# Kernel tuning notes

Measured on AMD Instinct MI355X. Metric: run time of the kernel, lower is better.

The kernel has to match this reference:

```python
import jax, jax.numpy as jnp
import numpy as np

HIDDEN = 1024
OUT = 16

def setup_inputs() -> dict:
    key = jax.random.key(0)
    ks = jax.random.split(key, 12)
    bs, hl, hf = 256, 256, 32
    T, ad = 64, 16
    flat = hl * hf
    s = lambda fi, fo: 1.0 / np.sqrt(fi)
    return {
        "history": jax.random.normal(ks[0], (bs, hl, hf), jnp.float32),
        "action": jax.random.normal(ks[1], (bs, T, ad), jnp.float32),
        # carry-init Dense layers (c and h)
        "Wc": jax.random.normal(ks[2], (flat, HIDDEN), jnp.float32) * s(flat, HIDDEN),
        "bc": jnp.zeros((HIDDEN,), jnp.float32),
        "Wh": jax.random.normal(ks[3], (flat, HIDDEN), jnp.float32) * s(flat, HIDDEN),
        "bh": jnp.zeros((HIDDEN,), jnp.float32),
        # LSTM cell: gates ordered [i, f, g, o]; input dense has no bias (flax LSTMCell)
        "Wi": jax.random.normal(ks[4], (ad, 4 * HIDDEN), jnp.float32) * s(ad, HIDDEN),
        "Wr": jax.random.normal(ks[5], (HIDDEN, 4 * HIDDEN), jnp.float32) * s(HIDDEN, HIDDEN),
        "bg": jnp.zeros((4 * HIDDEN,), jnp.float32),
        # output projection
        "Wo": jax.random.normal(ks[6], (HIDDEN, OUT), jnp.float32) * s(HIDDEN, OUT),
        "bo": jnp.zeros((OUT,), jnp.float32),
    }


def reference(history, action, Wc, bc, Wh, bh, Wi, Wr, bg, Wo, bo):
    bs = history.shape[0]
    flat = history.reshape(bs, -1)
    c0 = jax.nn.relu(flat @ Wc + bc)  # [bs, H]
    h0 = jax.nn.relu(flat @ Wh + bh)  # [bs, H]

    # precompute input contribution to gates for all steps: [T, bs, 4H]
    xg = jnp.einsum('bta,ag->tbg', action, Wi)

    def step(carry, xg_t):
        c, h = carry
        g = xg_t + h @ Wr + bg  # [bs, 4H]
        i, f, gg, o = jnp.split(g, 4, axis=-1)
        c = jax.nn.sigmoid(f) * c + jax.nn.sigmoid(i) * jnp.tanh(gg)
        h = jax.nn.sigmoid(o) * jnp.tanh(c)
        return (c, h), h

    _, hs = jax.lax.scan(step, (c0, h0), xg)  # hs: [T, bs, H]
    x = jnp.transpose(hs, (1, 0, 2))  # [bs, T, H]
    # Dropout is deterministic (identity)
    return x @ Wo + bo  # [bs, T, OUT]
```

## Files before the change

### kernel.cpp

```cpp
#include <hip/hip_runtime.h>
#include <math.h>

#define BS      256
#define FLAT    8192
#define H       1024
#define G4      4096
#define T_STEPS 64
#define AD      16
#define NOUT    16

typedef __attribute__((ext_vector_type(8))) short    bf16x8;
typedef __attribute__((ext_vector_type(4))) float    f32x4;
typedef __attribute__((ext_vector_type(8))) unsigned short u16x8;
typedef __attribute__((ext_vector_type(4))) unsigned short u16x4;

__device__ __forceinline__ float sigf(float x) { return 1.0f / (1.0f + __expf(-x)); }
__device__ __forceinline__ float tanh_fast(float x) {
    float a = fabsf(x);
    float e = __expf(-2.0f * a);
    float r = (1.0f - e) / (1.0f + e);
    return copysignf(r, x);
}
__device__ __forceinline__ unsigned short f2bf(float x) {
    unsigned int u = __float_as_uint(x);
    unsigned int r = (u + 0x7FFFu + ((u >> 16) & 1u)) >> 16;
    return (unsigned short)r;
}
__device__ __forceinline__ float bf2f(unsigned short u) {
    return __uint_as_float(((unsigned int)u) << 16);
}

#define OFF_WRP  (1u<<20)
#define OFF_WIP  (OFF_WRP + (8u<<20))
#define OFF_BGP  (OFF_WIP + (256u<<10))
#define OFF_HPA  (OFF_BGP + (16u<<10))
#define OFF_HPB  (OFF_HPA + (512u<<10))
#define OFF_HS   (OFF_HPB + (512u<<10))
#define OFF_PART (OFF_HS + 48u*BS*H*2u)

__global__ __launch_bounds__(256) void pack_wr(const float* __restrict__ Wr,
                                               unsigned short* __restrict__ Wp)
{
    int g  = blockIdx.x * 256 + threadIdx.x;
    int l  = g & 63;
    int nt = (g >> 6) & 3;
    int kc = (g >> 8) & 31;
    int nb = g >> 13;
    int col   = nt * 1024 + nb * 16 + (l & 15);
    int kbase = kc * 32 + (l >> 4) * 8;
    u16x8 o;
    #pragma unroll
    for (int i = 0; i < 8; ++i)
        o[i] = f2bf(Wr[(size_t)(kbase + i) * G4 + col]);
    *(u16x8*)&Wp[(size_t)g * 8] = o;
}

__global__ __launch_bounds__(256) void pack_wi(const float* __restrict__ Wi,
                                               unsigned short* __restrict__ Wp)
{
    int g  = blockIdx.x * 256 + threadIdx.x;
    int l  = g & 63;
    int nt = (g >> 6) & 3;
    int nb = g >> 8;
    int col   = nt * 1024 + nb * 16 + (l & 15);
    int kbase = (l >> 4) * 8;
    u16x8 o;
    #pragma unroll
    for (int i = 0; i < 8; ++i)
        o[i] = (kbase + i < AD) ? f2bf(Wi[(size_t)(kbase + i) * G4 + col]) : (unsigned short)0;
    *(u16x8*)&Wp[(size_t)g * 8] = o;
}

__global__ __launch_bounds__(256) void pack_bg(const float* __restrict__ bg,
                                               float* __restrict__ bgp)
{
    int t = blockIdx.x * 256 + threadIdx.x;
    int jj = t & 15, nt = (t >> 4) & 3, nb = t >> 6;
    bgp[t] = bg[nt * 1024 + nb * 16 + jj];
}

__global__ __launch_bounds__(256) void init_gemm_sk(
    const float* __restrict__ hist,
    const float* __restrict__ Wc, const float* __restrict__ Wh,
    float* __restrict__ partial)
{
    __shared__ float sA[32 * 34];
    __shared__ float sB[32 * 64];

    const int wg  = blockIdx.x;
    const int ks  = wg >> 8;
    const int mat = (wg >> 7) & 1;
    const int m   = wg & 127;
    const int r0  = (m >> 4) * 32;
    const int cc0 = (m & 15) * 64;
    const float* W = mat ? Wh : Wc;

    const int tid = threadIdx.x;
    const int tx  = tid & 15;
    const int ty  = tid >> 4;

    float acc[2][4] = {};
    const int kend = ks * 2048 + 2048;
    for (int k0 = ks * 2048; k0 < kend; k0 += 32) {
        {
            int kk = tid & 31, rr = tid >> 5;
            #pragma unroll
            for (int it = 0; it < 4; ++it) {
                int row = rr + it * 8;
                sA[kk * 34 + row] = hist[(size_t)(r0 + row) * FLAT + k0 + kk];
            }
        }
        {
            int col = tid & 63, kq = tid >> 6;
            #pragma unroll
            for (int it = 0; it < 8; ++it) {
                int k = kq + it * 4;
                sB[k * 64 + col] = W[(size_t)(k0 + k) * H + cc0 + col];
            }
        }
        __syncthreads();
        #pragma unroll
        for (int kk = 0; kk < 32; ++kk) {
            const float2 a2 = *(const float2*)&sA[kk * 34 + ty * 2];
            const float4 b4 = *(const float4*)&sB[kk * 64 + tx * 4];
            acc[0][0] = fmaf(a2.x, b4.x, acc[0][0]);
            acc[0][1] = fmaf(a2.x, b4.y, acc[0][1]);
            acc[0][2] = fmaf(a2.x, b4.z, acc[0][2]);
            acc[0][3] = fmaf(a2.x, b4.w, acc[0][3]);
            acc[1][0] = fmaf(a2.y, b4.x, acc[1][0]);
            acc[1][1] = fmaf(a2.y, b4.y, acc[1][1]);
            acc[1][2] = fmaf(a2.y, b4.z, acc[1][2]);
            acc[1][3] = fmaf(a2.y, b4.w, acc[1][3]);
        }
        __syncthreads();
    }

    float* dst = partial + (size_t)(ks * 2 + mat) * BS * H;
    #pragma unroll
    for (int i = 0; i < 2; ++i) {
        float4 o = { acc[i][0], acc[i][1], acc[i][2], acc[i][3] };
        *(float4*)&dst[(size_t)(r0 + ty * 2 + i) * H + cc0 + tx * 4] = o;
    }
}

__global__ __launch_bounds__(256) void reduce_pack(
    const float* __restrict__ partial,
    const float* __restrict__ bc, const float* __restrict__ bh,
    float* __restrict__ cbuf, unsigned short* __restrict__ hp0)
{
    int e = blockIdx.x * 256 + threadIdx.x;
    int mat = e >> 18;
    int rc  = e & 0x3FFFF;
    int row = rc >> 10, col = rc & 1023;
    float s = (mat ? bh : bc)[col];
    #pragma unroll
    for (int ks = 0; ks < 4; ++ks)
        s += partial[((size_t)(ks * 2 + mat) * BS + row) * H + col];
    s = fmaxf(s, 0.f);
    if (mat == 0) {
        cbuf[rc] = s;
    } else {
        int off = (row >> 6) * 65536 + (col >> 5) * 2048 + ((row >> 4) & 3) * 512
                + ((((col >> 3) & 3) << 4) + (row & 15)) * 8 + (col & 7);
        hp0[off] = f2bf(s);
    }
}

__global__ __launch_bounds__(256) void lstm_step(
    const float* __restrict__ act,
    const unsigned short* __restrict__ Wip,
    const unsigned short* __restrict__ Wrp,
    const float* __restrict__ bgp,
    const unsigned short* __restrict__ Aprev,
    unsigned short* __restrict__ Anext,
    float* __restrict__ cbuf,
    unsigned short* __restrict__ hs_t,
    int t)
{
    __shared__ __align__(16) unsigned short sB[2][4096];
    __shared__ __align__(16) unsigned short sAct[64 * 32];

    const int tid = threadIdx.x;
    const int wg  = blockIdx.x;
    const int mb  = wg >> 6;
    const int nb  = wg & 63;
    const int wv  = tid >> 6;
    const int l   = tid & 63;

    {
        int row = tid >> 2, q = tid & 3;
        float4 v = *(const float4*)&act[((size_t)(mb * 64 + row) * T_STEPS + t) * AD + q * 4];
        u16x4 b; b[0] = f2bf(v.x); b[1] = f2bf(v.y); b[2] = f2bf(v.z); b[3] = f2bf(v.w);
        *(u16x4*)&sAct[row * 32 + q * 4] = b;
        u16x4 z = { 0, 0, 0, 0 };
        *(u16x4*)&sAct[row * 32 + 16 + q * 4] = z;
    }

    const u16x8* Bsrc = (const u16x8*)(Wrp + (size_t)nb * 65536);
    {
        u16x8 s0 = Bsrc[tid], s1 = Bsrc[256 + tid];
        *(u16x8*)&sB[0][tid * 8]         = s0;
        *(u16x8*)&sB[0][(256 + tid) * 8] = s1;
    }
    u16x8 stg0 = Bsrc[512 + tid];
    u16x8 stg1 = Bsrc[768 + tid];

    const bf16x8* Asrc = ((const bf16x8*)Aprev) + mb * 8192 + wv * 64 + l;
    bf16x8 a0 = Asrc[0];
    bf16x8 a1 = Asrc[256];

    f32x4 acc[4];
    {
        const bf16x8* WiB = ((const bf16x8*)Wip) + nb * 256;
        bf16x8 wb0 = WiB[0 * 64 + l], wb1 = WiB[1 * 64 + l],
               wb2 = WiB[2 * 64 + l], wb3 = WiB[3 * 64 + l];
        float g0 = bgp[nb * 64 +  0 + (l & 15)];
        float g1 = bgp[nb * 64 + 16 + (l & 15)];
        float g2 = bgp[nb * 64 + 32 + (l & 15)];
        float g3 = bgp[nb * 64 + 48 + (l & 15)];
        acc[0] = (f32x4){ g0, g0, g0, g0 };
        acc[1] = (f32x4){ g1, g1, g1, g1 };
        acc[2] = (f32x4){ g2, g2, g2, g2 };
        acc[3] = (f32x4){ g3, g3, g3, g3 };

        __syncthreads();

        bf16x8 aa = *(const bf16x8*)&sAct[(wv * 16 + (l & 15)) * 32 + (l >> 4) * 8];
        acc[0] = __builtin_amdgcn_mfma_f32_16x16x32_bf16(aa, wb0, acc[0], 0, 0, 0);
        acc[1] = __builtin_amdgcn_mfma_f32_16x16x32_bf16(aa, wb1, acc[1], 0, 0, 0);
        acc[2] = __builtin_amdgcn_mfma_f32_16x16x32_bf16(aa, wb2, acc[2], 0, 0, 0);
        acc[3] = __builtin_amdgcn_mfma_f32_16x16x32_bf16(aa, wb3, acc[3], 0, 0, 0);
    }

    for (int c = 0; c < 16; ++c) {
        const int cb = c & 1;
        bf16x8 bf00 = *(const bf16x8*)&sB[cb][(0 * 64 + l) * 8];
        bf16x8 bf01 = *(const bf16x8*)&sB[cb][(1 * 64 + l) * 8];
        bf16x8 bf02 = *(const bf16x8*)&sB[cb][(2 * 64 + l) * 8];
        bf16x8 bf03 = *(const bf16x8*)&sB[cb][(3 * 64 + l) * 8];
        bf16x8 bf10 = *(const bf16x8*)&sB[cb][(4 * 64 + l) * 8];
        bf16x8 bf11 = *(const bf16x8*)&sB[cb][(5 * 64 + l) * 8];
        bf16x8 bf12 = *(const bf16x8*)&sB[cb][(6 * 64 + l) * 8];
        bf16x8 bf13 = *(const bf16x8*)&sB[cb][(7 * 64 + l) * 8];

        if (c < 15) {
            *(u16x8*)&sB[cb ^ 1][tid * 8]         = stg0;
            *(u16x8*)&sB[cb ^ 1][(256 + tid) * 8] = stg1;
        }
        if (c < 14) {
            stg0 = Bsrc[(c + 2) * 512 + tid];
            stg1 = Bsrc[(c + 2) * 512 + 256 + tid];
        }
        bf16x8 ca0 = a0, ca1 = a1;
        if (c < 15) {
            a0 = Asrc[(2 * (c + 1)) * 256];
            a1 = Asrc[(2 * (c + 1) + 1) * 256];
        }

        acc[0] = __builtin_amdgcn_mfma_f32_16x16x32_bf16(ca0, bf00, acc[0], 0, 0, 0);
        acc[1] = __builtin_amdgcn_mfma_f32_16x16x32_bf16(ca0, bf01, acc[1], 0, 0, 0);
        acc[2] = __builtin_amdgcn_mfma_f32_16x16x32_bf16(ca0, bf02, acc[2], 0, 0, 0);
        acc[3] = __builtin_amdgcn_mfma_f32_16x16x32_bf16(ca0, bf03, acc[3], 0, 0, 0);
        acc[0] = __builtin_amdgcn_mfma_f32_16x16x32_bf16(ca1, bf10, acc[0], 0, 0, 0);
        acc[1] = __builtin_amdgcn_mfma_f32_16x16x32_bf16(ca1, bf11, acc[1], 0, 0, 0);
        acc[2] = __builtin_amdgcn_mfma_f32_16x16x32_bf16(ca1, bf12, acc[2], 0, 0, 0);
        acc[3] = __builtin_amdgcn_mfma_f32_16x16x32_bf16(ca1, bf13, acc[3], 0, 0, 0);

        __syncthreads();
    }

    {
        const int jj   = l & 15;
        const int hid  = nb * 16 + jj;
        const int rowb = mb * 64 + wv * 16 + (l >> 4) * 4;
        const int kc   = nb >> 1;
        const int hgrp = ((nb & 1) << 1) | (jj >> 3);
        const int ii   = jj & 7;
        #pragma unroll
        for (int r = 0; r < 4; ++r) {
            int row = rowb + r;
            float gi = acc[0][r], gf = acc[1][r], gg = acc[2][r], go = acc[3][r];
            size_t off = (size_t)row * H + hid;
            float cv = sigf(gf) * cbuf[off] + sigf(gi) * tanh_fast(gg);
            cbuf[off] = cv;
            float hv = sigf(go) * tanh_fast(cv);
            unsigned short hb = f2bf(hv);
            hs_t[off] = hb;
            size_t poff = (size_t)mb * 65536 + kc * 2048 + wv * 512
                        + (hgrp * 16 + (row & 15)) * 8 + ii;
            Anext[poff] = hb;
        }
    }
}

__global__ __launch_bounds__(256) void out_proj(
    const unsigned short* __restrict__ hs,
    const float* __restrict__ Wo,
    const float* __restrict__ bo,
    float* __restrict__ out)
{
    __shared__ float sWo[H * NOUT];
    const int tid = threadIdx.x;
    for (int idx = tid; idx < H * NOUT; idx += 256) sWo[idx] = Wo[idx];
    __syncthreads();

    const int o    = tid & 15;
    const int pl   = tid >> 4;
    const int pair = blockIdx.x * 16 + pl;
    const int b    = pair >> 6;
    const int t    = pair & 63;
    const unsigned short* hrow = hs + ((size_t)t * BS + b) * H;

    float acc = bo[o];
    for (int k = 0; k < H; k += 8) {
        u16x8 u = *(const u16x8*)&hrow[k];
        #pragma unroll
        for (int j = 0; j < 8; ++j)
            acc = fmaf(bf2f(u[j]), sWo[(k + j) * 16 + o], acc);
    }
    out[(size_t)pair * 16 + o] = acc;
}

extern "C" void kernel_launch(void* const* d_in, const int* in_sizes, int n_in,
                              void* d_out, int out_size, void* d_ws, size_t ws_size,
                              hipStream_t stream)
{
    const float* hist = (const float*)d_in[0];
    const float* act  = (const float*)d_in[1];
    const float* Wc   = (const float*)d_in[2];
    const float* bc   = (const float*)d_in[3];
    const float* Wh   = (const float*)d_in[4];
    const float* bh   = (const float*)d_in[5];
    const float* Wi   = (const float*)d_in[6];
    const float* Wr   = (const float*)d_in[7];
    const float* bg   = (const float*)d_in[8];
    const float* Wo   = (const float*)d_in[9];
    const float* bo   = (const float*)d_in[10];
    float* out = (float*)d_out;

    char* W = (char*)d_ws;
    float*          cbuf = (float*)W;
    unsigned short* Wrp  = (unsigned short*)(W + OFF_WRP);
    unsigned short* Wip  = (unsigned short*)(W + OFF_WIP);
    float*          bgp  = (float*)(W + OFF_BGP);
    unsigned short* hpA  = (unsigned short*)(W + OFF_HPA);
    unsigned short* hpB  = (unsigned short*)(W + OFF_HPB);
    unsigned short* hs   = (unsigned short*)(W + OFF_HS);
    float*          part = (float*)(W + OFF_PART);

    pack_wr<<<dim3(2048), dim3(256), 0, stream>>>(Wr, Wrp);
    pack_wi<<<dim3(64),   dim3(256), 0, stream>>>(Wi, Wip);
    pack_bg<<<dim3(16),   dim3(256), 0, stream>>>(bg, bgp);

    init_gemm_sk<<<dim3(1024), dim3(256), 0, stream>>>(hist, Wc, Wh, part);
    reduce_pack<<<dim3(2048), dim3(256), 0, stream>>>(part, bc, bh, cbuf, hpA);

    for (int t = 0; t < T_STEPS; ++t) {
        const unsigned short* Ap = (t & 1) ? hpB : hpA;
        unsigned short*       An = (t & 1) ? hpA : hpB;
        lstm_step<<<dim3(256), dim3(256), 0, stream>>>(
            act, Wip, Wrp, bgp, Ap, An, cbuf, hs + (size_t)t * BS * H, t);
    }

    out_proj<<<dim3(1024), dim3(256), 0, stream>>>(hs, Wo, bo, out);
}
```

Before: 815.2 us.

## Move init GEMM to bf16 MFMA with packed operands and deepen LSTM A prefetch

Replaces the fp32 FMA split-K init GEMM for the c0/h0 carries with a bf16 MFMA kernel. The history and Wc/Wh operands are first packed into fragment-ordered layouts, and Bwp reuses the hs region because init finishes before the steps write to it. The action input is also pre-packed to bf16 once, so each lstm_step drops its shared-memory staging and one barrier. The step loop is unrolled by two so each parity keeps its own A registers, prefetching two chunks ahead. out_proj now handles four row groups per block. Risks are lower precision in the init GEMM and the extra packing kernels and memory traffic.

```diff
diff --git a/kernel.cpp b/kernel.cpp
--- a/kernel.cpp
+++ b/kernel.cpp
@@ -36,7 +36,9 @@
 #define OFF_HPA  (OFF_BGP + (16u<<10))
 #define OFF_HPB  (OFF_HPA + (512u<<10))
 #define OFF_HS   (OFF_HPB + (512u<<10))
-#define OFF_PART (OFF_HS + 48u*BS*H*2u)
+#define OFF_AHP  (OFF_HS + (32u<<20))
+#define OFF_AXP  (OFF_AHP + (4u<<20))
+#define OFF_PART (OFF_AXP + (1u<<20))
 
 __global__ __launch_bounds__(256) void pack_wr(const float* __restrict__ Wr,
                                                unsigned short* __restrict__ Wp)
@@ -79,95 +81,155 @@
     bgp[t] = bg[nt * 1024 + nb * 16 + jj];
 }
 
-__global__ __launch_bounds__(256) void init_gemm_sk(
-    const float* __restrict__ hist,
-    const float* __restrict__ Wc, const float* __restrict__ Wh,
-    float* __restrict__ partial)
-{
-    __shared__ float sA[32 * 34];
-    __shared__ float sB[32 * 64];
-
+__global__ __launch_bounds__(256) void pack_hist(const float* __restrict__ hist,
+                                                 unsigned short* __restrict__ Ap)
+{
+    int g  = blockIdx.x * 256 + threadIdx.x;
+    int l  = g & 63;
+    int kc = (g >> 6) & 255;
+    int mb = g >> 14;
+    const float* src = hist + (size_t)(mb * 16 + (l & 15)) * FLAT + kc * 32 + (l >> 4) * 8;
+    float4 v0 = *(const float4*)src;
+    float4 v1 = *(const float4*)(src + 4);
+    u16x8 o;
+    o[0]=f2bf(v0.x); o[1]=f2bf(v0.y); o[2]=f2bf(v0.z); o[3]=f2bf(v0.w);
+    o[4]=f2bf(v1.x); o[5]=f2bf(v1.y); o[6]=f2bf(v1.z); o[7]=f2bf(v1.w);
+    *(u16x8*)&Ap[(size_t)g * 8] = o;
+}
+
+__global__ __launch_bounds__(256) void pack_wb(const float* __restrict__ Wc,
+                                               const float* __restrict__ Wh,
+                                               unsigned short* __restrict__ Bp)
+{
+    int g  = blockIdx.x * 256 + threadIdx.x;
+    int l  = g & 63;
+    int kc = (g >> 6) & 255;
+    int nb = g >> 14;
+    const float* src = (nb & 64) ? Wh : Wc;
+    int n = (nb & 63) * 16 + (l & 15);
+    int k = kc * 32 + (l >> 4) * 8;
+    u16x8 o;
+    #pragma unroll
+    for (int i = 0; i < 8; ++i)
+        o[i] = f2bf(src[(size_t)(k + i) * H + n]);
+    *(u16x8*)&Bp[(size_t)g * 8] = o;
+}
+
+__global__ __launch_bounds__(256) void pack_act(const float* __restrict__ act,
+                                                unsigned short* __restrict__ Axp)
+{
+    int g = blockIdx.x * 256 + threadIdx.x;
+    int l = g & 63;
+    int q = (g >> 6) & 15;
+    int t = g >> 10;
+    int row = q * 16 + (l & 15);
+    int kb  = (l >> 4) * 8;
+    u16x8 o;
+    if (kb < AD) {
+        const float* src = act + ((size_t)row * T_STEPS + t) * AD + kb;
+        float4 v0 = *(const float4*)src;
+        float4 v1 = *(const float4*)(src + 4);
+        o[0]=f2bf(v0.x); o[1]=f2bf(v0.y); o[2]=f2bf(v0.z); o[3]=f2bf(v0.w);
+        o[4]=f2bf(v1.x); o[5]=f2bf(v1.y); o[6]=f2bf(v1.z); o[7]=f2bf(v1.w);
+    } else {
+        o = (u16x8){0,0,0,0,0,0,0,0};
+    }
+    *(u16x8*)&Axp[(size_t)g * 8] = o;
+}
+
+__global__ __launch_bounds__(256) void init_gemm_mfma(
+    const unsigned short* __restrict__ Ap,
+    const unsigned short* __restrict__ Bp,
+    float* __restrict__ part)
+{
     const int wg  = blockIdx.x;
-    const int ks  = wg >> 8;
-    const int mat = (wg >> 7) & 1;
-    const int m   = wg & 127;
-    const int r0  = (m >> 4) * 32;
-    const int cc0 = (m & 15) * 64;
-    const float* W = mat ? Wh : Wc;
-
+    const int mb  = wg & 3;
+    const int nbl = (wg >> 2) & 15;
+    const int ks  = wg >> 6;
     const int tid = threadIdx.x;
-    const int tx  = tid & 15;
-    const int ty  = tid >> 4;
-
-    float acc[2][4] = {};
-    const int kend = ks * 2048 + 2048;
-    for (int k0 = ks * 2048; k0 < kend; k0 += 32) {
-        {
-            int kk = tid & 31, rr = tid >> 5;
+    const int wv  = tid >> 6;
+    const int l   = tid & 63;
+    const int wm  = wv & 1;
+    const int wn  = wv >> 1;
+
+    const bf16x8* AV = (const bf16x8*)Ap;
+    const bf16x8* BV = (const bf16x8*)Bp;
+    const int am0 = mb * 4 + wm * 2;
+    const int bn0 = nbl * 8 + wn * 4;
+    const bf16x8* A0 = AV + (size_t)am0 * 16384 + l;
+    const bf16x8* A1 = A0 + 16384;
+    const bf16x8* B0 = BV + (size_t)bn0 * 16384 + l;
+    const bf16x8* B1 = B0 + 16384;
+    const bf16x8* B2 = B1 + 16384;
+    const bf16x8* B3 = B2 + 16384;
+
+    const int k0 = ks * 64;
+    f32x4 acc[2][4];
+    #pragma unroll
+    for (int m = 0; m < 2; ++m)
+        #pragma unroll
+        for (int n = 0; n < 4; ++n)
+            acc[m][n] = (f32x4){0.f, 0.f, 0.f, 0.f};
+
+    bf16x8 a0 = A0[(size_t)k0 * 64], a1 = A1[(size_t)k0 * 64];
+    bf16x8 b0 = B0[(size_t)k0 * 64], b1 = B1[(size_t)k0 * 64];
+    bf16x8 b2 = B2[(size_t)k0 * 64], b3 = B3[(size_t)k0 * 64];
+
+    for (int kc = k0; kc < k0 + 64; ++kc) {
+        bf16x8 na0, na1, nb0, nb1, nb2, nb3;
+        const bool more = (kc + 1) < k0 + 64;
+        if (more) {
+            size_t off = (size_t)(kc + 1) * 64;
+            na0 = A0[off]; na1 = A1[off];
+            nb0 = B0[off]; nb1 = B1[off]; nb2 = B2[off]; nb3 = B3[off];
+        }
+        acc[0][0] = __builtin_amdgcn_mfma_f32_16x16x32_bf16(a0, b0, acc[0][0], 0, 0, 0);
+        acc[0][1] = __builtin_amdgcn_mfma_f32_16x16x32_bf16(a0, b1, acc[0][1], 0, 0, 0);
+        acc[0][2] = __builtin_amdgcn_mfma_f32_16x16x32_bf16(a0, b2, acc[0][2], 0, 0, 0);
+        acc[0][3] = __builtin_amdgcn_mfma_f32_16x16x32_bf16(a0, b3, acc[0][3], 0, 0, 0);
+        acc[1][0] = __builtin_amdgcn_mfma_f32_16x16x32_bf16(a1, b0, acc[1][0], 0, 0, 0);
+        acc[1][1] = __builtin_amdgcn_mfma_f32_16x16x32_bf16(a1, b1, acc[1][1], 0, 0, 0);
+        acc[1][2] = __builtin_amdgcn_mfma_f32_16x16x32_bf16(a1, b2, acc[1][2], 0, 0, 0);
+        acc[1][3] = __builtin_amdgcn_mfma_f32_16x16x32_bf16(a1, b3, acc[1][3], 0, 0, 0);
+        if (more) { a0 = na0; a1 = na1; b0 = nb0; b1 = nb1; b2 = nb2; b3 = nb3; }
+    }
+
+    const int rbase = mb * 64 + wm * 32 + (l >> 4) * 4;
+    const int cbase = nbl * 128 + wn * 64 + (l & 15);
+    float* pdst = part + (size_t)ks * (BS * 2048);
+    #pragma unroll
+    for (int m = 0; m < 2; ++m)
+        #pragma unroll
+        for (int n = 0; n < 4; ++n)
             #pragma unroll
-            for (int it = 0; it < 4; ++it) {
-                int row = rr + it * 8;
-                sA[kk * 34 + row] = hist[(size_t)(r0 + row) * FLAT + k0 + kk];
-            }
-        }
-        {
-            int col = tid & 63, kq = tid >> 6;
-            #pragma unroll
-            for (int it = 0; it < 8; ++it) {
-                int k = kq + it * 4;
-                sB[k * 64 + col] = W[(size_t)(k0 + k) * H + cc0 + col];
-            }
-        }
-        __syncthreads();
-        #pragma unroll
-        for (int kk = 0; kk < 32; ++kk) {
-            const float2 a2 = *(const float2*)&sA[kk * 34 + ty * 2];
-            const float4 b4 = *(const float4*)&sB[kk * 64 + tx * 4];
-            acc[0][0] = fmaf(a2.x, b4.x, acc[0][0]);
-            acc[0][1] = fmaf(a2.x, b4.y, acc[0][1]);
-            acc[0][2] = fmaf(a2.x, b4.z, acc[0][2]);
-            acc[0][3] = fmaf(a2.x, b4.w, acc[0][3]);
-            acc[1][0] = fmaf(a2.y, b4.x, acc[1][0]);
-            acc[1][1] = fmaf(a2.y, b4.y, acc[1][1]);
-            acc[1][2] = fmaf(a2.y, b4.z, acc[1][2]);
-            acc[1][3] = fmaf(a2.y, b4.w, acc[1][3]);
-        }
-        __syncthreads();
-    }
-
-    float* dst = partial + (size_t)(ks * 2 + mat) * BS * H;
-    #pragma unroll
-    for (int i = 0; i < 2; ++i) {
-        float4 o = { acc[i][0], acc[i][1], acc[i][2], acc[i][3] };
-        *(float4*)&dst[(size_t)(r0 + ty * 2 + i) * H + cc0 + tx * 4] = o;
-    }
-}
-
-__global__ __launch_bounds__(256) void reduce_pack(
-    const float* __restrict__ partial,
+            for (int r = 0; r < 4; ++r)
+                pdst[(size_t)(rbase + m * 16 + r) * 2048 + cbase + n * 16] = acc[m][n][r];
+}
+
+__global__ __launch_bounds__(256) void init_reduce(
+    const float* __restrict__ part,
     const float* __restrict__ bc, const float* __restrict__ bh,
     float* __restrict__ cbuf, unsigned short* __restrict__ hp0)
 {
     int e = blockIdx.x * 256 + threadIdx.x;
-    int mat = e >> 18;
-    int rc  = e & 0x3FFFF;
-    int row = rc >> 10, col = rc & 1023;
-    float s = (mat ? bh : bc)[col];
+    int row = e >> 11, col = e & 2047;
+    float s = (col < 1024) ? bc[col] : bh[col - 1024];
     #pragma unroll
     for (int ks = 0; ks < 4; ++ks)
-        s += partial[((size_t)(ks * 2 + mat) * BS + row) * H + col];
+        s += part[(size_t)ks * (BS * 2048) + e];
     s = fmaxf(s, 0.f);
-    if (mat == 0) {
-        cbuf[rc] = s;
+    if (col < 1024) {
+        cbuf[(size_t)row * H + col] = s;
     } else {
-        int off = (row >> 6) * 65536 + (col >> 5) * 2048 + ((row >> 4) & 3) * 512
-                + ((((col >> 3) & 3) << 4) + (row & 15)) * 8 + (col & 7);
+        int hid = col - 1024;
+        int off = (row >> 6) * 65536 + (hid >> 5) * 2048 + ((row >> 4) & 3) * 512
+                + ((((hid >> 3) & 3) << 4) + (row & 15)) * 8 + (hid & 7);
         hp0[off] = f2bf(s);
     }
 }
 
 __global__ __launch_bounds__(256) void lstm_step(
-    const float* __restrict__ act,
+    const unsigned short* __restrict__ Axp,
     const unsigned short* __restrict__ Wip,
     const unsigned short* __restrict__ Wrp,
     const float* __restrict__ bgp,
@@ -178,7 +240,6 @@
     int t)
 {
     __shared__ __align__(16) unsigned short sB[2][4096];
-    __shared__ __align__(16) unsigned short sAct[64 * 32];
 
     const int tid = threadIdx.x;
     const int wg  = blockIdx.x;
@@ -187,15 +248,6 @@
     const int wv  = tid >> 6;
     const int l   = tid & 63;
 
-    {
-        int row = tid >> 2, q = tid & 3;
-        float4 v = *(const float4*)&act[((size_t)(mb * 64 + row) * T_STEPS + t) * AD + q * 4];
-        u16x4 b; b[0] = f2bf(v.x); b[1] = f2bf(v.y); b[2] = f2bf(v.z); b[3] = f2bf(v.w);
-        *(u16x4*)&sAct[row * 32 + q * 4] = b;
-        u16x4 z = { 0, 0, 0, 0 };
-        *(u16x4*)&sAct[row * 32 + 16 + q * 4] = z;
-    }
-
     const u16x8* Bsrc = (const u16x8*)(Wrp + (size_t)nb * 65536);
     {
         u16x8 s0 = Bsrc[tid], s1 = Bsrc[256 + tid];
@@ -206,8 +258,8 @@
     u16x8 stg1 = Bsrc[768 + tid];
 
     const bf16x8* Asrc = ((const bf16x8*)Aprev) + mb * 8192 + wv * 64 + l;
-    bf16x8 a0 = Asrc[0];
-    bf16x8 a1 = Asrc[256];
+    bf16x8 aE0 = Asrc[0],   aE1 = Asrc[256];
+    bf16x8 aO0 = Asrc[512], aO1 = Asrc[768];
 
     f32x4 acc[4];
     {
@@ -223,51 +275,52 @@
         acc[2] = (f32x4){ g2, g2, g2, g2 };
         acc[3] = (f32x4){ g3, g3, g3, g3 };
 
-        __syncthreads();
-
-        bf16x8 aa = *(const bf16x8*)&sAct[(wv * 16 + (l & 15)) * 32 + (l >> 4) * 8];
+        bf16x8 aa = *(((const bf16x8*)Axp) + ((size_t)t * 16 + mb * 4 + wv) * 64 + l);
         acc[0] = __builtin_amdgcn_mfma_f32_16x16x32_bf16(aa, wb0, acc[0], 0, 0, 0);
         acc[1] = __builtin_amdgcn_mfma_f32_16x16x32_bf16(aa, wb1, acc[1], 0, 0, 0);
         acc[2] = __builtin_amdgcn_mfma_f32_16x16x32_bf16(aa, wb2, acc[2], 0, 0, 0);
         acc[3] = __builtin_amdgcn_mfma_f32_16x16x32_bf16(aa, wb3, acc[3], 0, 0, 0);
     }
-
-    for (int c = 0; c < 16; ++c) {
-        const int cb = c & 1;
-        bf16x8 bf00 = *(const bf16x8*)&sB[cb][(0 * 64 + l) * 8];
-        bf16x8 bf01 = *(const bf16x8*)&sB[cb][(1 * 64 + l) * 8];
-        bf16x8 bf02 = *(const bf16x8*)&sB[cb][(2 * 64 + l) * 8];
-        bf16x8 bf03 = *(const bf16x8*)&sB[cb][(3 * 64 + l) * 8];
-        bf16x8 bf10 = *(const bf16x8*)&sB[cb][(4 * 64 + l) * 8];
-        bf16x8 bf11 = *(const bf16x8*)&sB[cb][(5 * 64 + l) * 8];
-        bf16x8 bf12 = *(const bf16x8*)&sB[cb][(6 * 64 + l) * 8];
-        bf16x8 bf13 = *(const bf16x8*)&sB[cb][(7 * 64 + l) * 8];
-
-        if (c < 15) {
-            *(u16x8*)&sB[cb ^ 1][tid * 8]         = stg0;
-            *(u16x8*)&sB[cb ^ 1][(256 + tid) * 8] = stg1;
-        }
-        if (c < 14) {
-            stg0 = Bsrc[(c + 2) * 512 + tid];
-            stg1 = Bsrc[(c + 2) * 512 + 256 + tid];
-        }
-        bf16x8 ca0 = a0, ca1 = a1;
-        if (c < 15) {
-            a0 = Asrc[(2 * (c + 1)) * 256];
-            a1 = Asrc[(2 * (c + 1) + 1) * 256];
-        }
-
-        acc[0] = __builtin_amdgcn_mfma_f32_16x16x32_bf16(ca0, bf00, acc[0], 0, 0, 0);
-        acc[1] = __builtin_amdgcn_mfma_f32_16x16x32_bf16(ca0, bf01, acc[1], 0, 0, 0);
-        acc[2] = __builtin_amdgcn_mfma_f32_16x16x32_bf16(ca0, bf02, acc[2], 0, 0, 0);
-        acc[3] = __builtin_amdgcn_mfma_f32_16x16x32_bf16(ca0, bf03, acc[3], 0, 0, 0);
-        acc[0] = __builtin_amdgcn_mfma_f32_16x16x32_bf16(ca1, bf10, acc[0], 0, 0, 0);
-        acc[1] = __builtin_amdgcn_mfma_f32_16x16x32_bf16(ca1, bf11, acc[1], 0, 0, 0);
-        acc[2] = __builtin_amdgcn_mfma_f32_16x16x32_bf16(ca1, bf12, acc[2], 0, 0, 0);
-        acc[3] = __builtin_amdgcn_mfma_f32_16x16x32_bf16(ca1, bf13, acc[3], 0, 0, 0);
-
-        __syncthreads();
-    }
+    __syncthreads();
+
+    #define CHUNK_BODY(C, CB, AX0, AX1)                                             \
+    {                                                                               \
+        bf16x8 n0, n1;                                                              \
+        if ((C) < 14) { n0 = Asrc[(2*(C)+4) * 256]; n1 = Asrc[(2*(C)+5) * 256]; }   \
+        bf16x8 bf00 = *(const bf16x8*)&sB[CB][(0 * 64 + l) * 8];                    \
+        bf16x8 bf01 = *(const bf16x8*)&sB[CB][(1 * 64 + l) * 8];                    \
+        bf16x8 bf02 = *(const bf16x8*)&sB[CB][(2 * 64 + l) * 8];                    \
+        bf16x8 bf03 = *(const bf16x8*)&sB[CB][(3 * 64 + l) * 8];                    \
+        bf16x8 bf10 = *(const bf16x8*)&sB[CB][(4 * 64 + l) * 8];                    \
+        bf16x8 bf11 = *(const bf16x8*)&sB[CB][(5 * 64 + l) * 8];                    \
+        bf16x8 bf12 = *(const bf16x8*)&sB[CB][(6 * 64 + l) * 8];                    \
+        bf16x8 bf13 = *(const bf16x8*)&sB[CB][(7 * 64 + l) * 8];                    \
+        if ((C) < 15) {                                                             \
+            *(u16x8*)&sB[(CB) ^ 1][tid * 8]         = stg0;                         \
+            *(u16x8*)&sB[(CB) ^ 1][(256 + tid) * 8] = stg1;                         \
+        }                                                                           \
+        if ((C) < 14) {                                                             \
+            stg0 = Bsrc[((C) + 2) * 512 + tid];                                     \
+            stg1 = Bsrc[((C) + 2) * 512 + 256 + tid];                               \
+        }                                                                           \
+        acc[0] = __builtin_amdgcn_mfma_f32_16x16x32_bf16(AX0, bf00, acc[0], 0,0,0); \
+        acc[1] = __builtin_amdgcn_mfma_f32_16x16x32_bf16(AX0, bf01, acc[1], 0,0,0); \
+        acc[2] = __builtin_amdgcn_mfma_f32_16x16x32_bf16(AX0, bf02, acc[2], 0,0,0); \
+        acc[3] = __builtin_amdgcn_mfma_f32_16x16x32_bf16(AX0, bf03, acc[3], 0,0,0); \
+        acc[0] = __builtin_amdgcn_mfma_f32_16x16x32_bf16(AX1, bf10, acc[0], 0,0,0); \
+        acc[1] = __builtin_amdgcn_mfma_f32_16x16x32_bf16(AX1, bf11, acc[1], 0,0,0); \
+        acc[2] = __builtin_amdgcn_mfma_f32_16x16x32_bf16(AX1, bf12, acc[2], 0,0,0); \
+        acc[3] = __builtin_amdgcn_mfma_f32_16x16x32_bf16(AX1, bf13, acc[3], 0,0,0); \
+        if ((C) < 14) { AX0 = n0; AX1 = n1; }                                       \
+        __syncthreads();                                                            \
+    }
+
+    for (int it = 0; it < 8; ++it) {
+        const int c0 = 2 * it;
+        CHUNK_BODY(c0,     0, aE0, aE1)
+        CHUNK_BODY(c0 + 1, 1, aO0, aO1)
+    }
+    #undef CHUNK_BODY
 
     {
         const int jj   = l & 15;
@@ -304,21 +357,24 @@
     for (int idx = tid; idx < H * NOUT; idx += 256) sWo[idx] = Wo[idx];
     __syncthreads();
 
-    const int o    = tid & 15;
-    const int pl   = tid >> 4;
-    const int pair = blockIdx.x * 16 + pl;
-    const int b    = pair >> 6;
-    const int t    = pair & 63;
-    const unsigned short* hrow = hs + ((size_t)t * BS + b) * H;
-
-    float acc = bo[o];
-    for (int k = 0; k < H; k += 8) {
-        u16x8 u = *(const u16x8*)&hrow[k];
-        #pragma unroll
-        for (int j = 0; j < 8; ++j)
-            acc = fmaf(bf2f(u[j]), sWo[(k + j) * 16 + o], acc);
-    }
-    out[(size_t)pair * 16 + o] = acc;
+    const int o  = tid & 15;
+    const int pl = tid >> 4;
+    const float bias = bo[o];
+    #pragma unroll
+    for (int pass = 0; pass < 4; ++pass) {
+        const int pair = blockIdx.x * 64 + pass * 16 + pl;
+        const int b = pair >> 6;
+        const int t = pair & 63;
+        const unsigned short* hrow = hs + ((size_t)t * BS + b) * H;
+        float acc = bias;
+        for (int k = 0; k < H; k += 8) {
+            u16x8 u = *(const u16x8*)&hrow[k];
+            #pragma unroll
+            for (int j = 0; j < 8; ++j)
+                acc = fmaf(bf2f(u[j]), sWo[(k + j) * 16 + o], acc);
+        }
+        out[(size_t)pair * 16 + o] = acc;
+    }
 }
 
 extern "C" void kernel_launch(void* const* d_in, const int* in_sizes, int n_in,
@@ -346,21 +402,27 @@
     unsigned short* hpA  = (unsigned short*)(W + OFF_HPA);
     unsigned short* hpB  = (unsigned short*)(W + OFF_HPB);
     unsigned short* hs   = (unsigned short*)(W + OFF_HS);
+    unsigned short* Bwp  = (unsigned short*)(W + OFF_HS);
+    unsigned short* Ahp  = (unsigned short*)(W + OFF_AHP);
+    unsigned short* Axp  = (unsigned short*)(W + OFF_AXP);
     float*          part = (float*)(W + OFF_PART);
 
-    pack_wr<<<dim3(2048), dim3(256), 0, stream>>>(Wr, Wrp);
-    pack_wi<<<dim3(64),   dim3(256), 0, stream>>>(Wi, Wip);
-    pack_bg<<<dim3(16),   dim3(256), 0, stream>>>(bg, bgp);
-
-    init_gemm_sk<<<dim3(1024), dim3(256), 0, stream>>>(hist, Wc, Wh, part);
-    reduce_pack<<<dim3(2048), dim3(256), 0, stream>>>(part, bc, bh, cbuf, hpA);
+    pack_wr  <<<dim3(2048), dim3(256), 0, stream>>>(Wr, Wrp);
+    pack_wi  <<<dim3(64),   dim3(256), 0, stream>>>(Wi, Wip);
+    pack_bg  <<<dim3(16),   dim3(256), 0, stream>>>(bg, bgp);
+    pack_hist<<<dim3(1024), dim3(256), 0, stream>>>(hist, Ahp);
+    pack_wb  <<<dim3(8192), dim3(256), 0, stream>>>(Wc, Wh, Bwp);
+    pack_act <<<dim3(256),  dim3(256), 0, stream>>>(act, Axp);
+
+    init_gemm_mfma<<<dim3(256), dim3(256), 0, stream>>>(Ahp, Bwp, part);
+    init_reduce  <<<dim3(2048), dim3(256), 0, stream>>>(part, bc, bh, cbuf, hpA);
 
     for (int t = 0; t < T_STEPS; ++t) {
         const unsigned short* Ap = (t & 1) ? hpB : hpA;
         unsigned short*       An = (t & 1) ? hpA : hpB;
         lstm_step<<<dim3(256), dim3(256), 0, stream>>>(
-            act, Wip, Wrp, bgp, Ap, An, cbuf, hs + (size_t)t * BS * H, t);
-    }
-
-    out_proj<<<dim3(1024), dim3(256), 0, stream>>>(hs, Wo, bo, out);
-}
+            Axp, Wip, Wrp, bgp, Ap, An, cbuf, hs + (size_t)t * BS * H, t);
+    }
+
+    out_proj<<<dim3(256), dim3(256), 0, stream>>>(hs, Wo, bo, out);
+}
```

Result: faster. 729.5 us (-10.5%).
